# Performance work log

Hardware: AMD Instinct MI355X
Metric: run time of the kernel (lower is better)

Reference implementation:

```python
import jax, jax.numpy as jnp
import numpy as np

B, T, D, K = 8, 4096, 1024, 4096

def setup_inputs() -> dict:
    key = jax.random.key(0)
    kx, kc = jax.random.split(key)
    x = jax.random.normal(kx, (B, T, D), dtype=jnp.float32)
    C = jax.random.normal(kc, (D, K), dtype=jnp.float32)  # centroids stored as [d, K]
    Cnorm = jnp.sum(C * C, axis=0, keepdims=True)  # [1, K], matches torch precompute
    return {"x": x, "C": C, "Cnorm": Cnorm}

def reference(x, C, Cnorm):
    batched = x.ndim == 3
    if batched:
        b, t, d = x.shape
        x2 = x.reshape(-1, d)  # [N, d]
    else:
        x2 = x
    dist = jnp.sum(x2 * x2, axis=1, keepdims=True) - 2.0 * (x2 @ C) + Cnorm
    assigned = jnp.argmin(dist, axis=1)
    if batched:
        assigned = assigned.reshape(b, t)
    return assigned
```

## Files before the change

kernel.cpp:

```cpp
#include <hip/hip_runtime.h>
#include <cstdint>
#include <cstddef>

typedef _Float16 half8 __attribute__((ext_vector_type(8)));
typedef _Float16 half4 __attribute__((ext_vector_type(4)));
typedef float    floatx4 __attribute__((ext_vector_type(4)));

constexpr int N_ROWS = 32768;
constexpr int D_DIM  = 1024;
constexpr int K_CENT = 4096;
constexpr int CAP    = 4096;
constexpr int KSL    = 2;
constexpr int RSL    = 8;
constexpr float EPS_GAP = 0.4f;

__device__ __forceinline__ void gload_lds16(const void* g, void* l) {
    __builtin_amdgcn_global_load_lds(
        (const __attribute__((address_space(1))) uint32_t*)g,
        (__attribute__((address_space(3))) uint32_t*)l, 16, 0, 0);
}

__global__ __launch_bounds__(256) void convert_C_kernel(
    const float* __restrict__ C, _Float16* __restrict__ ChiT, _Float16* __restrict__ CloT)
{
    __shared__ float tile[32][33];
    const int bk = blockIdx.x, bd = blockIdx.y, t = threadIdx.x;
    const int r = t >> 3, c4 = (t & 7) * 4;
    const float4 v = *(const float4*)&C[(size_t)(bd * 32 + r) * K_CENT + bk * 32 + c4];
    tile[r][c4 + 0] = v.x; tile[r][c4 + 1] = v.y;
    tile[r][c4 + 2] = v.z; tile[r][c4 + 3] = v.w;
    __syncthreads();
    half4 h, l;
#pragma unroll
    for (int i = 0; i < 4; ++i) {
        const float f = tile[c4 + i][r];
        const _Float16 hi = (_Float16)f;
        h[i] = hi;
        l[i] = (_Float16)(f - (float)hi);
    }
    *(half4*)&ChiT[(size_t)(bk * 32 + r) * D_DIM + bd * 32 + c4] = h;
    *(half4*)&CloT[(size_t)(bk * 32 + r) * D_DIM + bd * 32 + c4] = l;
}

__global__ __launch_bounds__(256) void convert_x_kernel(
    const float* __restrict__ x, _Float16* __restrict__ xh)
{
    const size_t g = (size_t)blockIdx.x * 256 + threadIdx.x;
    const float4 v0 = *(const float4*)&x[g * 8];
    const float4 v1 = *(const float4*)&x[g * 8 + 4];
    half8 h;
    h[0] = (_Float16)v0.x; h[1] = (_Float16)v0.y; h[2] = (_Float16)v0.z; h[3] = (_Float16)v0.w;
    h[4] = (_Float16)v1.x; h[5] = (_Float16)v1.y; h[6] = (_Float16)v1.z; h[7] = (_Float16)v1.w;
    *(half8*)&xh[g * 8] = h;
}

constexpr int P_XH = 0;
constexpr int P_CH = 4096;
constexpr int P_HB = 12288;

__device__ __forceinline__ void stage6(
    _Float16* buf, const _Float16* __restrict__ xh, const _Float16* __restrict__ ChiT,
    int row0, int kc, int kd, int wid, int scol, int skg)
{
#pragma unroll
    for (int q = 0; q < 2; ++q) {
        const int sub = wid * 2 + q;
        gload_lds16(&xh[(size_t)(row0 + sub * 16 + scol) * D_DIM + kd + skg * 8],
                    buf + P_XH + sub * 512);
    }
#pragma unroll
    for (int q = 0; q < 4; ++q) {
        const int sub = wid * 4 + q;
        gload_lds16(&ChiT[(size_t)(kc + sub * 16 + scol) * D_DIM + kd + skg * 8],
                    buf + P_CH + sub * 512);
    }
}

__global__ __launch_bounds__(256, 2) void kmeans_pass1(
    const _Float16* __restrict__ xh, const _Float16* __restrict__ ChiT,
    const float* __restrict__ Cnorm,
    float* __restrict__ m1buf, int* __restrict__ i1buf, float* __restrict__ m2buf)
{
    __shared__ _Float16 lds[3][P_HB];
    __shared__ float red_d[2][64][2];
    __shared__ int   red_i[2][64][2];
    __shared__ float red_2[2][64][2];

    const int bid  = blockIdx.x;
    const int xcd  = bid & 7;
    const int ks   = xcd & 1;
    const int rb   = (bid >> 3) * 4 + (xcd >> 1);
    const int row0 = rb * 128;
    const int kb0  = ks * (K_CENT / KSL);

    const int tid  = threadIdx.x;
    const int lane = tid & 63;
    const int wid  = tid >> 6;
    const int wm   = wid >> 1;
    const int wn   = wid & 1;

    const int l15 = lane & 15;
    const int l4  = lane >> 4;
    const int kge = l4 ^ ((l15 >> 1) & 3);
    const int fragoff = l15 * 32 + kge * 8;

    const int scol = lane >> 2;
    const int skg  = (lane & 3) ^ ((scol >> 1) & 3);

    float rm1 = 3.4e38f, rm2 = 3.4e38f;
    int   ri1 = 0;

    constexpr int NSTEP = ((K_CENT / KSL) / 256) * 32;

    stage6(lds[0], xh, ChiT, row0, kb0, 0,  wid, scol, skg);
    stage6(lds[1], xh, ChiT, row0, kb0, 32, wid, scol, skg);

    floatx4 acc[4][8];
#pragma unroll
    for (int i = 0; i < 4; ++i)
#pragma unroll
        for (int j = 0; j < 8; ++j) acc[i][j] = (floatx4)0.0f;

    int cur = 0;
    for (int s = 0; s < NSTEP; ++s) {
        _Float16* bufc = lds[cur];
        const int s2 = s + 2;
        if (s2 < NSTEP) {
            const int nkc = kb0 + (s2 >> 5) * 256;
            const int nkd = (s2 & 31) * 32;
            const int b2  = (cur >= 1) ? cur - 1 : 2;
            stage6(lds[b2], xh, ChiT, row0, nkc, nkd, wid, scol, skg);
            asm volatile("s_waitcnt vmcnt(12)" ::: "memory");
        } else if (s + 1 < NSTEP) {
            asm volatile("s_waitcnt vmcnt(6)" ::: "memory");
        } else {
            asm volatile("s_waitcnt vmcnt(0)" ::: "memory");
        }
        __builtin_amdgcn_s_barrier();
        __builtin_amdgcn_sched_barrier(0);

        half8 ah[4], bh[8];
#pragma unroll
        for (int i = 0; i < 4; ++i)
            ah[i] = *(const half8*)(bufc + P_XH + (wm * 4 + i) * 512 + fragoff);
#pragma unroll
        for (int j = 0; j < 8; ++j)
            bh[j] = *(const half8*)(bufc + P_CH + (wn * 8 + j) * 512 + fragoff);

        __builtin_amdgcn_s_setprio(1);
#pragma unroll
        for (int i = 0; i < 4; ++i)
#pragma unroll
            for (int j = 0; j < 8; ++j)
                acc[i][j] = __builtin_amdgcn_mfma_f32_16x16x32_f16(ah[i], bh[j], acc[i][j], 0, 0, 0);
        __builtin_amdgcn_s_setprio(0);

        __builtin_amdgcn_sched_barrier(0);
        asm volatile("" ::: "memory");
        __builtin_amdgcn_s_barrier();

        cur = (cur == 2) ? 0 : cur + 1;

        if ((s & 31) == 31) {
            const int ci   = s >> 5;
            const int colw = ci * 256 + wn * 128;
            float cn8[8];
#pragma unroll
            for (int j = 0; j < 8; ++j) cn8[j] = Cnorm[kb0 + colw + j * 16 + l15];

#pragma unroll
            for (int i = 0; i < 4; ++i)
#pragma unroll
                for (int r = 0; r < 4; ++r) {
                    float m1 = 3.4e38f, m2 = 3.4e38f;
                    int   i1 = 0;
#pragma unroll
                    for (int j = 0; j < 8; ++j) {
                        const float d  = fmaf(-2.0f, acc[i][j][r], cn8[j]);
                        const int   ix = kb0 + colw + j * 16 + l15;
                        if (d < m1) { m2 = m1; m1 = d; i1 = ix; }
                        else if (d < m2) { m2 = d; }
                    }
#pragma unroll
                    for (int off = 1; off < 16; off <<= 1) {
                        const float om1 = __shfl_xor(m1, off, 64);
                        const int   oi  = __shfl_xor(i1, off, 64);
                        const float om2 = __shfl_xor(m2, off, 64);
                        const float nm2 = fminf(fminf(m2, om2), fmaxf(m1, om1));
                        if (om1 < m1 || (om1 == m1 && oi < i1)) { m1 = om1; i1 = oi; }
                        m2 = nm2;
                    }
                    if (l15 == 0) {
                        const int rr = i * 16 + l4 * 4 + r;
                        red_d[wm][rr][wn] = m1;
                        red_i[wm][rr][wn] = i1;
                        red_2[wm][rr][wn] = m2;
                    }
                }
            asm volatile("s_waitcnt lgkmcnt(0)" ::: "memory");
            __builtin_amdgcn_s_barrier();
            __builtin_amdgcn_sched_barrier(0);

            if (tid < 128) {
                const int hh = tid >> 7;
                const int rr = tid & 127;
                const int h2 = rr >> 6;
                const int r2 = rr & 63;
                float m1 = red_d[h2][r2][0], m2 = red_2[h2][r2][0];
                int   i1 = red_i[h2][r2][0];
                const float om1 = red_d[h2][r2][1];
                const int   oi  = red_i[h2][r2][1];
                const float om2 = red_2[h2][r2][1];
                m2 = fminf(fminf(m2, om2), fmaxf(m1, om1));
                if (om1 < m1 || (om1 == m1 && oi < i1)) { m1 = om1; i1 = oi; }
                const float nm2 = fminf(fminf(rm2, m2), fmaxf(rm1, m1));
                if (m1 < rm1 || (m1 == rm1 && i1 < ri1)) { rm1 = m1; ri1 = i1; }
                rm2 = nm2;
                (void)hh;
            }

#pragma unroll
            for (int i = 0; i < 4; ++i)
#pragma unroll
                for (int j = 0; j < 8; ++j) acc[i][j] = (floatx4)0.0f;
        }
    }

    if (tid < 128) {
        const size_t off = (size_t)ks * N_ROWS + row0 + tid;
        m1buf[off] = rm1;
        i1buf[off] = ri1;
        m2buf[off] = rm2;
    }
}

__global__ __launch_bounds__(256) void kmeans_merge4(
    const float* __restrict__ m1buf, const int* __restrict__ i1buf,
    const float* __restrict__ m2buf, int* __restrict__ out,
    int* __restrict__ urows, unsigned int* __restrict__ ucount)
{
    const int row = blockIdx.x * 256 + threadIdx.x;
    float m1 = m1buf[row], m2 = m2buf[row];
    int   i1 = i1buf[row];
#pragma unroll
    for (int s = 1; s < KSL; ++s) {
        const float om1 = m1buf[(size_t)s * N_ROWS + row];
        const float om2 = m2buf[(size_t)s * N_ROWS + row];
        const int   oi  = i1buf[(size_t)s * N_ROWS + row];
        const float nm2 = fminf(fminf(m2, om2), fmaxf(m1, om1));
        if (om1 < m1 || (om1 == m1 && oi < i1)) { m1 = om1; i1 = oi; }
        m2 = nm2;
    }
    out[row] = i1;
    if (m2 - m1 <= EPS_GAP) {
        const unsigned slot = atomicAdd(ucount, 1u);
        if (slot < (unsigned)CAP) urows[slot] = row;
    }
}

__global__ __launch_bounds__(64) void kmeans_gather(
    const float* __restrict__ x, const int* __restrict__ urows,
    const unsigned int* __restrict__ ucount,
    _Float16* __restrict__ xch, _Float16* __restrict__ xcl)
{
    const unsigned cntr = *ucount;
    const unsigned cnt = cntr > (unsigned)CAP ? (unsigned)CAP : cntr;
    const unsigned slot = blockIdx.x;
    if (slot >= cnt) return;
    const int row = urows[slot];
    const int t = threadIdx.x;
#pragma unroll
    for (int e = 0; e < 16; ++e) {
        const int idx = e * 64 + t;
        const float v = x[(size_t)row * D_DIM + idx];
        const _Float16 h = (_Float16)v;
        xch[(size_t)slot * D_DIM + idx] = h;
        xcl[(size_t)slot * D_DIM + idx] = (_Float16)(v - (float)h);
    }
}

constexpr int R_XH = 0;
constexpr int R_XL = 1024;
constexpr int R_CH = 2048;
constexpr int R_CL = 10240;
constexpr int R_HB = 18432;

__global__ __launch_bounds__(256) void kmeans_rescore2(
    const _Float16* __restrict__ xch, const _Float16* __restrict__ xcl,
    const _Float16* __restrict__ ChiT, const _Float16* __restrict__ CloT,
    const float* __restrict__ Cnorm, const unsigned int* __restrict__ ucount,
    float* __restrict__ rpd, int* __restrict__ rpi)
{
    const unsigned cntr = *ucount;
    const unsigned cnt = cntr > (unsigned)CAP ? (unsigned)CAP : cntr;
    const int bid = blockIdx.x;
    const int ksl = bid & 7;
    const int grp = bid >> 3;
    if ((unsigned)(grp * 32) >= cnt) return;

    __shared__ _Float16 lds[2][R_HB];
    __shared__ float rd[32][4];
    __shared__ int   ri[32][4];

    const int tid  = threadIdx.x;
    const int lane = tid & 63;
    const int wid  = tid >> 6;
    const int l15  = lane & 15;
    const int l4   = lane >> 4;
    const int kge  = l4 ^ ((l15 >> 1) & 3);
    const int fragoff = l15 * 32 + kge * 8;
    const int scol = lane >> 2;
    const int skg  = (lane & 3) ^ ((scol >> 1) & 3);

    const int base  = grp * 32;
    const int kbase = ksl * (K_CENT / RSL);

    float best[2][4];
    int   bidx[2][4];
#pragma unroll
    for (int i = 0; i < 2; ++i)
#pragma unroll
        for (int r = 0; r < 4; ++r) { best[i][r] = 3.4e38f; bidx[i][r] = 0; }

    for (int ch = 0; ch < 2; ++ch) {
        const int kc = kbase + ch * 256;
        floatx4 acc[2][4];
#pragma unroll
        for (int i = 0; i < 2; ++i)
#pragma unroll
            for (int j = 0; j < 4; ++j) acc[i][j] = (floatx4)0.0f;

        {
            _Float16* buf = lds[0];
#pragma unroll
            for (int q = 0; q < 4; ++q) {
                const int sub = wid * 4 + q;
                gload_lds16(&ChiT[(size_t)(kc + sub * 16 + scol) * D_DIM + 0 + skg * 8], buf + R_CH + sub * 512);
                gload_lds16(&CloT[(size_t)(kc + sub * 16 + scol) * D_DIM + 0 + skg * 8], buf + R_CL + sub * 512);
            }
            if (wid < 2)
                gload_lds16(&xch[(size_t)(base + wid * 16 + scol) * D_DIM + 0 + skg * 8], buf + R_XH + wid * 512);
            else
                gload_lds16(&xcl[(size_t)(base + (wid - 2) * 16 + scol) * D_DIM + 0 + skg * 8], buf + R_XL + (wid - 2) * 512);
            __syncthreads();
        }

        for (int kdi = 0; kdi < D_DIM / 32; ++kdi) {
            const int cur = kdi & 1;
            _Float16* bufc = lds[cur];
            _Float16* bufn = lds[cur ^ 1];
            const int  kdn = (kdi + 1) * 32;
            const bool pf  = (kdi + 1 < D_DIM / 32);

            if (pf) {
#pragma unroll
                for (int q = 0; q < 4; ++q) {
                    const int sub = wid * 4 + q;
                    gload_lds16(&ChiT[(size_t)(kc + sub * 16 + scol) * D_DIM + kdn + skg * 8], bufn + R_CH + sub * 512);
                    gload_lds16(&CloT[(size_t)(kc + sub * 16 + scol) * D_DIM + kdn + skg * 8], bufn + R_CL + sub * 512);
                }
                if (wid < 2)
                    gload_lds16(&xch[(size_t)(base + wid * 16 + scol) * D_DIM + kdn + skg * 8], bufn + R_XH + wid * 512);
                else
                    gload_lds16(&xcl[(size_t)(base + (wid - 2) * 16 + scol) * D_DIM + kdn + skg * 8], bufn + R_XL + (wid - 2) * 512);
            }

            half8 ah[2], al[2], bh[4], bl[4];
#pragma unroll
            for (int i = 0; i < 2; ++i) {
                ah[i] = *(const half8*)(bufc + R_XH + i * 512 + fragoff);
                al[i] = *(const half8*)(bufc + R_XL + i * 512 + fragoff);
            }
#pragma unroll
            for (int j = 0; j < 4; ++j) {
                bh[j] = *(const half8*)(bufc + R_CH + (wid * 4 + j) * 512 + fragoff);
                bl[j] = *(const half8*)(bufc + R_CL + (wid * 4 + j) * 512 + fragoff);
            }
#pragma unroll
            for (int i = 0; i < 2; ++i)
#pragma unroll
                for (int j = 0; j < 4; ++j) {
                    acc[i][j] = __builtin_amdgcn_mfma_f32_16x16x32_f16(ah[i], bh[j], acc[i][j], 0, 0, 0);
                    acc[i][j] = __builtin_amdgcn_mfma_f32_16x16x32_f16(ah[i], bl[j], acc[i][j], 0, 0, 0);
                    acc[i][j] = __builtin_amdgcn_mfma_f32_16x16x32_f16(al[i], bh[j], acc[i][j], 0, 0, 0);
                }
            __syncthreads();
        }

#pragma unroll
        for (int j = 0; j < 4; ++j) {
            const int col = kc + wid * 64 + j * 16 + l15;
            const float cn = Cnorm[col];
#pragma unroll
            for (int i = 0; i < 2; ++i)
#pragma unroll
                for (int r = 0; r < 4; ++r) {
                    const float d = fmaf(-2.0f, acc[i][j][r], cn);
                    if (d < best[i][r]) { best[i][r] = d; bidx[i][r] = col; }
                }
        }
    }

#pragma unroll
    for (int i = 0; i < 2; ++i)
#pragma unroll
        for (int r = 0; r < 4; ++r) {
            float m1 = best[i][r];
            int   i1 = bidx[i][r];
#pragma unroll
            for (int off = 1; off < 16; off <<= 1) {
                const float om1 = __shfl_xor(m1, off, 64);
                const int   oi  = __shfl_xor(i1, off, 64);
                if (om1 < m1 || (om1 == m1 && oi < i1)) { m1 = om1; i1 = oi; }
            }
            if (l15 == 0) { rd[i * 16 + l4 * 4 + r][wid] = m1; ri[i * 16 + l4 * 4 + r][wid] = i1; }
        }
    __syncthreads();

    if (tid < 32) {
        float m1 = rd[tid][0];
        int   i1 = ri[tid][0];
#pragma unroll
        for (int w = 1; w < 4; ++w) {
            const float om1 = rd[tid][w];
            const int   oi  = ri[tid][w];
            if (om1 < m1 || (om1 == m1 && oi < i1)) { m1 = om1; i1 = oi; }
        }
        rpd[(size_t)(base + tid) * RSL + ksl] = m1;
        rpi[(size_t)(base + tid) * RSL + ksl] = i1;
    }
}

__global__ __launch_bounds__(256) void kmeans_merge2(
    const float* __restrict__ rpd, const int* __restrict__ rpi,
    const int* __restrict__ urows, const unsigned int* __restrict__ ucount,
    int* __restrict__ out)
{
    const unsigned cntr = *ucount;
    const unsigned cnt = cntr > (unsigned)CAP ? (unsigned)CAP : cntr;
    const unsigned s = blockIdx.x * 256 + threadIdx.x;
    if (s >= cnt) return;
    float m1 = rpd[(size_t)s * RSL];
    int   i1 = rpi[(size_t)s * RSL];
#pragma unroll
    for (int k = 1; k < RSL; ++k) {
        const float om = rpd[(size_t)s * RSL + k];
        const int   oi = rpi[(size_t)s * RSL + k];
        if (om < m1 || (om == m1 && oi < i1)) { m1 = om; i1 = oi; }
    }
    out[urows[s]] = i1;
}

constexpr int F_XH = 0, F_XL = 4096, F_CH = 8192, F_CL = 16384, F_HB = 24576;

__device__ __forceinline__ void write_x2(_Float16* buf, const float4 v, int r, int kb) {
    const _Float16 h0 = (_Float16)v.x, h1 = (_Float16)v.y;
    const _Float16 h2 = (_Float16)v.z, h3 = (_Float16)v.w;
    const int kg  = kb >> 3;
    const int hs  = (kb >> 2) & 1;
    const int kge = kg ^ ((r >> 1) & 3);
    const int base = (r >> 4) * 512 + (r & 15) * 32 + kge * 8 + hs * 4;
    *(half4*)(buf + F_XH + base) = (half4){h0, h1, h2, h3};
    *(half4*)(buf + F_XL + base) = (half4){(_Float16)(v.x - (float)h0), (_Float16)(v.y - (float)h1),
                                           (_Float16)(v.z - (float)h2), (_Float16)(v.w - (float)h3)};
}

__global__ __launch_bounds__(512, 2) void kmeans_mfma_kernel(
    const float* __restrict__ x, const _Float16* __restrict__ ChiT,
    const _Float16* __restrict__ CloT, const float* __restrict__ Cnorm,
    int* __restrict__ out)
{
    __shared__ _Float16 lds[2][F_HB];
    __shared__ float red_d[2][64][4];
    __shared__ int   red_i[2][64][4];

    const int tid  = threadIdx.x;
    const int lane = tid & 63;
    const int wid  = tid >> 6;
    const int wm   = wid >> 2;
    const int wn   = wid & 3;
    const int row0 = blockIdx.x * 128;
    const int l15 = lane & 15;
    const int l4  = lane >> 4;
    const int kge = l4 ^ ((l15 >> 1) & 3);
    const int fragoff = l15 * 32 + kge * 8;
    const int sr = tid >> 2, sc = tid & 3;
    const int ccol = lane >> 2;
    const int ckg  = (lane & 3) ^ ((ccol >> 1) & 3);

    float best[4][4];
    int   bidx[4][4];
#pragma unroll
    for (int i = 0; i < 4; ++i)
#pragma unroll
        for (int r = 0; r < 4; ++r) { best[i][r] = 3.4e38f; bidx[i][r] = 0; }

    for (int kc = 0; kc < K_CENT; kc += 256) {
        floatx4 acc[4][4];
#pragma unroll
        for (int i = 0; i < 4; ++i)
#pragma unroll
            for (int j = 0; j < 4; ++j) acc[i][j] = (floatx4)0.0f;
        {
            _Float16* buf = lds[0];
            const float4 xv0 = *(const float4*)&x[(size_t)(row0 + sr) * D_DIM + 0 + sc * 4];
            const float4 xv1 = *(const float4*)&x[(size_t)(row0 + sr) * D_DIM + 16 + sc * 4];
            gload_lds16(&ChiT[(size_t)(kc + wid * 16 + ccol) * D_DIM + 0 + ckg * 8], buf + F_CH + wid * 512);
            gload_lds16(&ChiT[(size_t)(kc + (wid + 8) * 16 + ccol) * D_DIM + 0 + ckg * 8], buf + F_CH + (wid + 8) * 512);
            gload_lds16(&CloT[(size_t)(kc + wid * 16 + ccol) * D_DIM + 0 + ckg * 8], buf + F_CL + wid * 512);
            gload_lds16(&CloT[(size_t)(kc + (wid + 8) * 16 + ccol) * D_DIM + 0 + ckg * 8], buf + F_CL + (wid + 8) * 512);
            write_x2(buf, xv0, sr, sc * 4);
            write_x2(buf, xv1, sr, sc * 4 + 16);
            __syncthreads();
        }
        for (int kdi = 0; kdi < D_DIM / 32; ++kdi) {
            const int cur = kdi & 1;
            _Float16* bufc = lds[cur];
            _Float16* bufn = lds[cur ^ 1];
            const int  kdn = (kdi + 1) * 32;
            const bool pf  = (kdi + 1 < D_DIM / 32);
            float4 xv0, xv1;
            if (pf) {
                xv0 = *(const float4*)&x[(size_t)(row0 + sr) * D_DIM + kdn + sc * 4];
                xv1 = *(const float4*)&x[(size_t)(row0 + sr) * D_DIM + kdn + 16 + sc * 4];
                gload_lds16(&ChiT[(size_t)(kc + wid * 16 + ccol) * D_DIM + kdn + ckg * 8], bufn + F_CH + wid * 512);
                gload_lds16(&ChiT[(size_t)(kc + (wid + 8) * 16 + ccol) * D_DIM + kdn + ckg * 8], bufn + F_CH + (wid + 8) * 512);
                gload_lds16(&CloT[(size_t)(kc + wid * 16 + ccol) * D_DIM + kdn + ckg * 8], bufn + F_CL + wid * 512);
                gload_lds16(&CloT[(size_t)(kc + (wid + 8) * 16 + ccol) * D_DIM + kdn + ckg * 8], bufn + F_CL + (wid + 8) * 512);
            }
            half8 ah[4], al[4], bh[4], bl[4];
#pragma unroll
            for (int i = 0; i < 4; ++i) {
                ah[i] = *(const half8*)(bufc + F_XH + (wm * 4 + i) * 512 + fragoff);
                al[i] = *(const half8*)(bufc + F_XL + (wm * 4 + i) * 512 + fragoff);
            }
#pragma unroll
            for (int j = 0; j < 4; ++j) {
                bh[j] = *(const half8*)(bufc + F_CH + (wn * 4 + j) * 512 + fragoff);
                bl[j] = *(const half8*)(bufc + F_CL + (wn * 4 + j) * 512 + fragoff);
            }
#pragma unroll
            for (int i = 0; i < 4; ++i)
#pragma unroll
                for (int j = 0; j < 4; ++j) {
                    acc[i][j] = __builtin_amdgcn_mfma_f32_16x16x32_f16(ah[i], bh[j], acc[i][j], 0, 0, 0);
                    acc[i][j] = __builtin_amdgcn_mfma_f32_16x16x32_f16(ah[i], bl[j], acc[i][j], 0, 0, 0);
                    acc[i][j] = __builtin_amdgcn_mfma_f32_16x16x32_f16(al[i], bh[j], acc[i][j], 0, 0, 0);
                }
            if (pf) {
                write_x2(bufn, xv0, sr, sc * 4);
                write_x2(bufn, xv1, sr, sc * 4 + 16);
            }
            __syncthreads();
        }
        const int colw = kc + wn * 64;
#pragma unroll
        for (int ns = 0; ns < 4; ++ns) {
            const float cn = Cnorm[colw + ns * 16 + l15];
            const int   ix = colw + ns * 16 + l15;
#pragma unroll
            for (int i = 0; i < 4; ++i)
#pragma unroll
                for (int r = 0; r < 4; ++r) {
                    const float d = fmaf(-2.0f, acc[i][ns][r], cn);
                    if (d < best[i][r]) { best[i][r] = d; bidx[i][r] = ix; }
                }
        }
    }
#pragma unroll
    for (int i = 0; i < 4; ++i)
#pragma unroll
        for (int r = 0; r < 4; ++r) {
            float d  = best[i][r];
            int   ix = bidx[i][r];
#pragma unroll
            for (int off = 1; off < 16; off <<= 1) {
                const float od = __shfl_xor(d, off, 64);
                const int   oi = __shfl_xor(ix, off, 64);
                if (od < d || (od == d && oi < ix)) { d = od; ix = oi; }
            }
            if (l15 == 0) {
                red_d[wm][i * 16 + l4 * 4 + r][wn] = d;
                red_i[wm][i * 16 + l4 * 4 + r][wn] = ix;
            }
        }
    __syncthreads();
    if (tid < 128) {
        const int hh = tid >> 6, rr = tid & 63;
        float bd = red_d[hh][rr][0];
        int   bi2 = red_i[hh][rr][0];
#pragma unroll
        for (int w = 1; w < 4; ++w) {
            const float od = red_d[hh][rr][w];
            const int   oi = red_i[hh][rr][w];
            if (od < bd || (od == bd && oi < bi2)) { bd = od; bi2 = oi; }
        }
        out[row0 + tid] = bi2;
    }
}

__global__ __launch_bounds__(256, 2) void kmeans_assign_f32(
    const float* __restrict__ x, const float* __restrict__ Cm,
    const float* __restrict__ Cnorm, int* __restrict__ out)
{
    __shared__ float xs[32][64];
    __shared__ float cs[32][64];
    const int tid = threadIdx.x;
    const int tx = tid & 15, ty = tid >> 4;
    const int row0 = blockIdx.x * 64;
    const int xr = tid >> 3, xc = tid & 7;
    const int cr = tid >> 4, cc = tid & 15;
    float best[4]; int bidx[4];
#pragma unroll
    for (int i = 0; i < 4; ++i) { best[i] = 3.4e38f; bidx[i] = 0; }
    for (int kc = 0; kc < K_CENT; kc += 64) {
        float acc[16];
#pragma unroll
        for (int i = 0; i < 16; ++i) acc[i] = 0.0f;
        for (int kd = 0; kd < D_DIM; kd += 32) {
            const float4 xv0 = *(const float4*)&x[(size_t)(row0 + xr) * D_DIM + kd + xc * 4];
            const float4 xv1 = *(const float4*)&x[(size_t)(row0 + xr + 32) * D_DIM + kd + xc * 4];
            const float4 cv0 = *(const float4*)&Cm[(size_t)(kd + cr) * K_CENT + kc + cc * 4];
            const float4 cv1 = *(const float4*)&Cm[(size_t)(kd + cr + 16) * K_CENT + kc + cc * 4];
            __syncthreads();
            xs[xc*4+0][xr] = xv0.x; xs[xc*4+1][xr] = xv0.y; xs[xc*4+2][xr] = xv0.z; xs[xc*4+3][xr] = xv0.w;
            xs[xc*4+0][xr+32] = xv1.x; xs[xc*4+1][xr+32] = xv1.y; xs[xc*4+2][xr+32] = xv1.z; xs[xc*4+3][xr+32] = xv1.w;
            *(float4*)&cs[cr][cc*4]    = cv0;
            *(float4*)&cs[cr+16][cc*4] = cv1;
            __syncthreads();
#pragma unroll
            for (int kk = 0; kk < 32; ++kk) {
                const float4 a = *(const float4*)&xs[kk][ty*4];
                const float4 b = *(const float4*)&cs[kk][tx*4];
                acc[ 0] += a.x*b.x; acc[ 1] += a.x*b.y; acc[ 2] += a.x*b.z; acc[ 3] += a.x*b.w;
                acc[ 4] += a.y*b.x; acc[ 5] += a.y*b.y; acc[ 6] += a.y*b.z; acc[ 7] += a.y*b.w;
                acc[ 8] += a.z*b.x; acc[ 9] += a.z*b.y; acc[10] += a.z*b.z; acc[11] += a.z*b.w;
                acc[12] += a.w*b.x; acc[13] += a.w*b.y; acc[14] += a.w*b.z; acc[15] += a.w*b.w;
            }
        }
        const float4 cn = *(const float4*)&Cnorm[kc + tx*4];
        const float cnv[4] = {cn.x, cn.y, cn.z, cn.w};
#pragma unroll
        for (int i = 0; i < 4; ++i)
#pragma unroll
            for (int j = 0; j < 4; ++j) {
                const float dist = cnv[j] - 2.0f * acc[i*4+j];
                const int   idx  = kc + tx*4 + j;
                if (dist < best[i]) { best[i] = dist; bidx[i] = idx; }
            }
    }
#pragma unroll
    for (int i = 0; i < 4; ++i) {
        float d = best[i]; int ix = bidx[i];
#pragma unroll
        for (int off = 1; off < 16; off <<= 1) {
            const float od = __shfl_xor(d, off, 64);
            const int   oi = __shfl_xor(ix, off, 64);
            if (od < d || (od == d && oi < ix)) { d = od; ix = oi; }
        }
        if (tx == 0) out[row0 + ty*4 + i] = ix;
    }
}

extern "C" void kernel_launch(void* const* d_in, const int* in_sizes, int n_in,
                              void* d_out, int out_size, void* d_ws, size_t ws_size,
                              hipStream_t stream) {
    const float* x     = (const float*)d_in[0];
    const float* C     = (const float*)d_in[1];
    const float* Cnorm = (const float*)d_in[2];
    int* out = (int*)d_out;

    const size_t chalf = (size_t)K_CENT * D_DIM;
    const size_t capd  = (size_t)CAP * D_DIM;
    const size_t xhN   = (size_t)N_ROWS * D_DIM;

    const size_t sz_base = (2 * chalf + 2 * capd) * 2
                         + (size_t)KSL * N_ROWS * 12
                         + (size_t)CAP * RSL * 8
                         + (size_t)CAP * 4 + 64;
    const size_t need_full = sz_base + xhN * 2;
    const size_t need_r3   = 2 * chalf * 2;

    if (ws_size >= need_full) {
        _Float16* ChiT = (_Float16*)d_ws;
        _Float16* CloT = ChiT + chalf;
        _Float16* xch  = CloT + chalf;
        _Float16* xcl  = xch + capd;
        float* m1buf = (float*)(xcl + capd);
        float* m2buf = m1buf + (size_t)KSL * N_ROWS;
        int*   i1buf = (int*)(m2buf + (size_t)KSL * N_ROWS);
        float* rpd   = (float*)(i1buf + (size_t)KSL * N_ROWS);
        int*   rpi   = (int*)(rpd + (size_t)CAP * RSL);
        int*   urows = rpi + (size_t)CAP * RSL;
        unsigned int* ucount = (unsigned int*)(urows + CAP);
        _Float16* xh = (_Float16*)(ucount + 16);

        convert_C_kernel<<<dim3(128, 32), 256, 0, stream>>>(C, ChiT, CloT);
        convert_x_kernel<<<dim3((int)(xhN / 2048)), 256, 0, stream>>>(x, xh);
        hipMemsetAsync(ucount, 0, sizeof(unsigned int), stream);
        kmeans_pass1<<<dim3(256 * KSL), 256, 0, stream>>>(xh, ChiT, Cnorm, m1buf, i1buf, m2buf);
        kmeans_merge4<<<dim3(N_ROWS / 256), 256, 0, stream>>>(m1buf, i1buf, m2buf, out, urows, ucount);
        kmeans_gather<<<dim3(CAP), 64, 0, stream>>>(x, urows, ucount, xch, xcl);
        kmeans_rescore2<<<dim3((CAP / 32) * RSL), 256, 0, stream>>>(xch, xcl, ChiT, CloT, Cnorm, ucount, rpd, rpi);
        kmeans_merge2<<<dim3(CAP / 256), 256, 0, stream>>>(rpd, rpi, urows, ucount, out);
    } else if (ws_size >= need_r3) {
        _Float16* ChiT = (_Float16*)d_ws;
        _Float16* CloT = ChiT + chalf;
        convert_C_kernel<<<dim3(128, 32), 256, 0, stream>>>(C, ChiT, CloT);
        kmeans_mfma_kernel<<<dim3(N_ROWS / 128), 512, 0, stream>>>(x, ChiT, CloT, Cnorm, out);
    } else {
        kmeans_assign_f32<<<dim3(N_ROWS / 64), 256, 0, stream>>>(x, C, Cnorm, out);
    }
}
```

Baseline: 476.2 us.

## Enlarge pass1 tile to 256x256 with 8 waves and split-phase staging

The first-pass GEMM kernel now uses 512-thread blocks, each covering 256 rows by 256 centroids per chunk, with 8 waves arranged 2x4 and each wave computing 128x64. The MFMA work per step is split into two halves. The x-tile and C-tile global-to-LDS loads are issued in separate phases between those halves, so loads overlap with compute. The larger tile raises arithmetic intensity and cuts redundant global/LDS traffic per output. In exchange there are more barriers per step, larger LDS use (three 32KB buffers), and half as many blocks (256), which may underfill the GPU.

Result: slower. 509.4 us (+7.0%).

```diff
diff --git a/kernel.cpp b/kernel.cpp
--- a/kernel.cpp
+++ b/kernel.cpp
@@ -54,50 +54,55 @@
     *(half8*)&xh[g * 8] = h;
 }
 
-constexpr int P_XH = 0;
-constexpr int P_CH = 4096;
-constexpr int P_HB = 12288;
-
-__device__ __forceinline__ void stage6(
-    _Float16* buf, const _Float16* __restrict__ xh, const _Float16* __restrict__ ChiT,
-    int row0, int kc, int kd, int wid, int scol, int skg)
+constexpr int P8_B  = 8192;
+constexpr int P8_HB = 16384;
+
+__device__ __forceinline__ void stageA8(
+    _Float16* buf, const _Float16* __restrict__ xh,
+    int row0, int kd, int wid, int scol, int skg)
 {
 #pragma unroll
     for (int q = 0; q < 2; ++q) {
         const int sub = wid * 2 + q;
         gload_lds16(&xh[(size_t)(row0 + sub * 16 + scol) * D_DIM + kd + skg * 8],
-                    buf + P_XH + sub * 512);
-    }
-#pragma unroll
-    for (int q = 0; q < 4; ++q) {
-        const int sub = wid * 4 + q;
+                    buf + sub * 512);
+    }
+}
+
+__device__ __forceinline__ void stageB8(
+    _Float16* buf, const _Float16* __restrict__ ChiT,
+    int kc, int kd, int wid, int scol, int skg)
+{
+#pragma unroll
+    for (int q = 0; q < 2; ++q) {
+        const int sub = wid * 2 + q;
         gload_lds16(&ChiT[(size_t)(kc + sub * 16 + scol) * D_DIM + kd + skg * 8],
-                    buf + P_CH + sub * 512);
-    }
-}
-
-__global__ __launch_bounds__(256, 2) void kmeans_pass1(
+                    buf + P8_B + sub * 512);
+    }
+}
+
+__global__ __launch_bounds__(512, 2) void kmeans_pass1(
     const _Float16* __restrict__ xh, const _Float16* __restrict__ ChiT,
     const float* __restrict__ Cnorm,
     float* __restrict__ m1buf, int* __restrict__ i1buf, float* __restrict__ m2buf)
 {
-    __shared__ _Float16 lds[3][P_HB];
-    __shared__ float red_d[2][64][2];
-    __shared__ int   red_i[2][64][2];
-    __shared__ float red_2[2][64][2];
+    __shared__ _Float16 lds[3][P8_HB];
+    __shared__ float red_d[256][4];
+    __shared__ int   red_i[256][4];
+    __shared__ float red_2[256][4];
 
     const int bid  = blockIdx.x;
     const int xcd  = bid & 7;
     const int ks   = xcd & 1;
     const int rb   = (bid >> 3) * 4 + (xcd >> 1);
-    const int row0 = rb * 128;
+    const int row0 = rb * 256;
     const int kb0  = ks * (K_CENT / KSL);
 
     const int tid  = threadIdx.x;
     const int lane = tid & 63;
     const int wid  = tid >> 6;
-    const int wm   = wid >> 1;
-    const int wn   = wid & 1;
+    const int wm   = wid >> 2;
+    const int wn   = wid & 3;
 
     const int l15 = lane & 15;
     const int l4  = lane >> 4;
@@ -110,123 +115,138 @@
     float rm1 = 3.4e38f, rm2 = 3.4e38f;
     int   ri1 = 0;
 
-    constexpr int NSTEP = ((K_CENT / KSL) / 256) * 32;
-
-    stage6(lds[0], xh, ChiT, row0, kb0, 0,  wid, scol, skg);
-    stage6(lds[1], xh, ChiT, row0, kb0, 32, wid, scol, skg);
-
-    floatx4 acc[4][8];
-#pragma unroll
-    for (int i = 0; i < 4; ++i)
-#pragma unroll
-        for (int j = 0; j < 8; ++j) acc[i][j] = (floatx4)0.0f;
+    constexpr int NCH   = (K_CENT / KSL) / 256;
+    constexpr int NSTEP = NCH * 32;
+
+    stageA8(lds[0], xh,   row0, 0,  wid, scol, skg);
+    stageB8(lds[0], ChiT, kb0,  0,  wid, scol, skg);
+    stageA8(lds[1], xh,   row0, 32, wid, scol, skg);
+    stageB8(lds[1], ChiT, kb0,  32, wid, scol, skg);
+    asm volatile("s_waitcnt vmcnt(4)" ::: "memory");
+    __builtin_amdgcn_s_barrier();
 
     int cur = 0;
-    for (int s = 0; s < NSTEP; ++s) {
-        _Float16* bufc = lds[cur];
-        const int s2 = s + 2;
-        if (s2 < NSTEP) {
-            const int nkc = kb0 + (s2 >> 5) * 256;
-            const int nkd = (s2 & 31) * 32;
-            const int b2  = (cur >= 1) ? cur - 1 : 2;
-            stage6(lds[b2], xh, ChiT, row0, nkc, nkd, wid, scol, skg);
-            asm volatile("s_waitcnt vmcnt(12)" ::: "memory");
-        } else if (s + 1 < NSTEP) {
-            asm volatile("s_waitcnt vmcnt(6)" ::: "memory");
-        } else {
-            asm volatile("s_waitcnt vmcnt(0)" ::: "memory");
-        }
+    int sg  = 0;
+
+    for (int ci = 0; ci < NCH; ++ci) {
+        floatx4 acc[8][4];
+#pragma unroll
+        for (int i = 0; i < 8; ++i)
+#pragma unroll
+            for (int j = 0; j < 4; ++j) acc[i][j] = (floatx4)0.0f;
+
+        for (int kdi = 0; kdi < 32; ++kdi, ++sg) {
+            _Float16* bufc = lds[cur];
+            const int  nb  = (cur == 0) ? 2 : cur - 1;
+            const int  s2  = sg + 2;
+            const bool st  = (s2 < NSTEP);
+            const int  kc2 = kb0 + (s2 >> 5) * 256;
+            const int  kd2 = (s2 & 31) * 32;
+
+            half8 ah[4], bh[4];
+#pragma unroll
+            for (int i = 0; i < 4; ++i)
+                ah[i] = *(const half8*)(bufc + (wm * 8 + i) * 512 + fragoff);
+#pragma unroll
+            for (int j = 0; j < 4; ++j)
+                bh[j] = *(const half8*)(bufc + P8_B + (wn * 4 + j) * 512 + fragoff);
+            if (st) stageA8(lds[nb], xh, row0, kd2, wid, scol, skg);
+
+            __builtin_amdgcn_s_barrier();
+            asm volatile("s_waitcnt lgkmcnt(0)" ::: "memory");
+            __builtin_amdgcn_sched_barrier(0);
+            __builtin_amdgcn_s_setprio(1);
+#pragma unroll
+            for (int i = 0; i < 4; ++i)
+#pragma unroll
+                for (int j = 0; j < 4; ++j)
+                    acc[i][j] = __builtin_amdgcn_mfma_f32_16x16x32_f16(ah[i], bh[j], acc[i][j], 0, 0, 0);
+            __builtin_amdgcn_s_setprio(0);
+            __builtin_amdgcn_sched_barrier(0);
+            __builtin_amdgcn_s_barrier();
+
+            half8 ah2[4];
+#pragma unroll
+            for (int i = 0; i < 4; ++i)
+                ah2[i] = *(const half8*)(bufc + (wm * 8 + 4 + i) * 512 + fragoff);
+            if (st) {
+                stageB8(lds[nb], ChiT, kc2, kd2, wid, scol, skg);
+                asm volatile("s_waitcnt vmcnt(4)" ::: "memory");
+            } else {
+                asm volatile("s_waitcnt vmcnt(0)" ::: "memory");
+            }
+            __builtin_amdgcn_s_barrier();
+            asm volatile("s_waitcnt lgkmcnt(0)" ::: "memory");
+            __builtin_amdgcn_sched_barrier(0);
+            __builtin_amdgcn_s_setprio(1);
+#pragma unroll
+            for (int i = 0; i < 4; ++i)
+#pragma unroll
+                for (int j = 0; j < 4; ++j)
+                    acc[4 + i][j] = __builtin_amdgcn_mfma_f32_16x16x32_f16(ah2[i], bh[j], acc[4 + i][j], 0, 0, 0);
+            __builtin_amdgcn_s_setprio(0);
+            __builtin_amdgcn_sched_barrier(0);
+            __builtin_amdgcn_s_barrier();
+
+            cur = (cur == 2) ? 0 : cur + 1;
+        }
+
+        const int colw = ci * 256 + wn * 64;
+        float cn4[4];
+#pragma unroll
+        for (int j = 0; j < 4; ++j) cn4[j] = Cnorm[kb0 + colw + j * 16 + l15];
+
+#pragma unroll
+        for (int i = 0; i < 8; ++i)
+#pragma unroll
+            for (int r = 0; r < 4; ++r) {
+                float m1 = 3.4e38f, m2 = 3.4e38f;
+                int   i1 = 0;
+#pragma unroll
+                for (int j = 0; j < 4; ++j) {
+                    const float d  = fmaf(-2.0f, acc[i][j][r], cn4[j]);
+                    const int   ix = kb0 + colw + j * 16 + l15;
+                    if (d < m1) { m2 = m1; m1 = d; i1 = ix; }
+                    else if (d < m2) { m2 = d; }
+                }
+#pragma unroll
+                for (int off = 1; off < 16; off <<= 1) {
+                    const float om1 = __shfl_xor(m1, off, 64);
+                    const int   oi  = __shfl_xor(i1, off, 64);
+                    const float om2 = __shfl_xor(m2, off, 64);
+                    const float nm2 = fminf(fminf(m2, om2), fmaxf(m1, om1));
+                    if (om1 < m1 || (om1 == m1 && oi < i1)) { m1 = om1; i1 = oi; }
+                    m2 = nm2;
+                }
+                if (l15 == 0) {
+                    const int rr = wm * 128 + i * 16 + l4 * 4 + r;
+                    red_d[rr][wn] = m1;
+                    red_i[rr][wn] = i1;
+                    red_2[rr][wn] = m2;
+                }
+            }
+        asm volatile("s_waitcnt lgkmcnt(0)" ::: "memory");
         __builtin_amdgcn_s_barrier();
         __builtin_amdgcn_sched_barrier(0);
 
-        half8 ah[4], bh[8];
-#pragma unroll
-        for (int i = 0; i < 4; ++i)
-            ah[i] = *(const half8*)(bufc + P_XH + (wm * 4 + i) * 512 + fragoff);
-#pragma unroll
-        for (int j = 0; j < 8; ++j)
-            bh[j] = *(const half8*)(bufc + P_CH + (wn * 8 + j) * 512 + fragoff);
-
-        __builtin_amdgcn_s_setprio(1);
-#pragma unroll
-        for (int i = 0; i < 4; ++i)
-#pragma unroll
-            for (int j = 0; j < 8; ++j)
-                acc[i][j] = __builtin_amdgcn_mfma_f32_16x16x32_f16(ah[i], bh[j], acc[i][j], 0, 0, 0);
-        __builtin_amdgcn_s_setprio(0);
-
-        __builtin_amdgcn_sched_barrier(0);
-        asm volatile("" ::: "memory");
-        __builtin_amdgcn_s_barrier();
-
-        cur = (cur == 2) ? 0 : cur + 1;
-
-        if ((s & 31) == 31) {
-            const int ci   = s >> 5;
-            const int colw = ci * 256 + wn * 128;
-            float cn8[8];
-#pragma unroll
-            for (int j = 0; j < 8; ++j) cn8[j] = Cnorm[kb0 + colw + j * 16 + l15];
-
-#pragma unroll
-            for (int i = 0; i < 4; ++i)
-#pragma unroll
-                for (int r = 0; r < 4; ++r) {
-                    float m1 = 3.4e38f, m2 = 3.4e38f;
-                    int   i1 = 0;
-#pragma unroll
-                    for (int j = 0; j < 8; ++j) {
-                        const float d  = fmaf(-2.0f, acc[i][j][r], cn8[j]);
-                        const int   ix = kb0 + colw + j * 16 + l15;
-                        if (d < m1) { m2 = m1; m1 = d; i1 = ix; }
-                        else if (d < m2) { m2 = d; }
-                    }
-#pragma unroll
-                    for (int off = 1; off < 16; off <<= 1) {
-                        const float om1 = __shfl_xor(m1, off, 64);
-                        const int   oi  = __shfl_xor(i1, off, 64);
-                        const float om2 = __shfl_xor(m2, off, 64);
-                        const float nm2 = fminf(fminf(m2, om2), fmaxf(m1, om1));
-                        if (om1 < m1 || (om1 == m1 && oi < i1)) { m1 = om1; i1 = oi; }
-                        m2 = nm2;
-                    }
-                    if (l15 == 0) {
-                        const int rr = i * 16 + l4 * 4 + r;
-                        red_d[wm][rr][wn] = m1;
-                        red_i[wm][rr][wn] = i1;
-                        red_2[wm][rr][wn] = m2;
-                    }
-                }
-            asm volatile("s_waitcnt lgkmcnt(0)" ::: "memory");
-            __builtin_amdgcn_s_barrier();
-            __builtin_amdgcn_sched_barrier(0);
-
-            if (tid < 128) {
-                const int hh = tid >> 7;
-                const int rr = tid & 127;
-                const int h2 = rr >> 6;
-                const int r2 = rr & 63;
-                float m1 = red_d[h2][r2][0], m2 = red_2[h2][r2][0];
-                int   i1 = red_i[h2][r2][0];
-                const float om1 = red_d[h2][r2][1];
-                const int   oi  = red_i[h2][r2][1];
-                const float om2 = red_2[h2][r2][1];
+        if (tid < 256) {
+            float m1 = red_d[tid][0], m2 = red_2[tid][0];
+            int   i1 = red_i[tid][0];
+#pragma unroll
+            for (int w = 1; w < 4; ++w) {
+                const float om1 = red_d[tid][w];
+                const int   oi  = red_i[tid][w];
+                const float om2 = red_2[tid][w];
                 m2 = fminf(fminf(m2, om2), fmaxf(m1, om1));
                 if (om1 < m1 || (om1 == m1 && oi < i1)) { m1 = om1; i1 = oi; }
-                const float nm2 = fminf(fminf(rm2, m2), fmaxf(rm1, m1));
-                if (m1 < rm1 || (m1 == rm1 && i1 < ri1)) { rm1 = m1; ri1 = i1; }
-                rm2 = nm2;
-                (void)hh;
-            }
-
-#pragma unroll
-            for (int i = 0; i < 4; ++i)
-#pragma unroll
-                for (int j = 0; j < 8; ++j) acc[i][j] = (floatx4)0.0f;
-        }
-    }
-
-    if (tid < 128) {
+            }
+            const float nm2 = fminf(fminf(rm2, m2), fmaxf(rm1, m1));
+            if (m1 < rm1 || (m1 == rm1 && i1 < ri1)) { rm1 = m1; ri1 = i1; }
+            rm2 = nm2;
+        }
+    }
+
+    if (tid < 256) {
         const size_t off = (size_t)ks * N_ROWS + row0 + tid;
         m1buf[off] = rm1;
         i1buf[off] = ri1;
@@ -698,7 +718,7 @@
         convert_C_kernel<<<dim3(128, 32), 256, 0, stream>>>(C, ChiT, CloT);
         convert_x_kernel<<<dim3((int)(xhN / 2048)), 256, 0, stream>>>(x, xh);
         hipMemsetAsync(ucount, 0, sizeof(unsigned int), stream);
-        kmeans_pass1<<<dim3(256 * KSL), 256, 0, stream>>>(xh, ChiT, Cnorm, m1buf, i1buf, m2buf);
+        kmeans_pass1<<<dim3(128 * KSL), 512, 0, stream>>>(xh, ChiT, Cnorm, m1buf, i1buf, m2buf);
         kmeans_merge4<<<dim3(N_ROWS / 256), 256, 0, stream>>>(m1buf, i1buf, m2buf, out, urows, ucount);
         kmeans_gather<<<dim3(CAP), 64, 0, stream>>>(x, urows, ucount, xch, xcl);
         kmeans_rescore2<<<dim3((CAP / 32) * RSL), 256, 0, stream>>>(xch, xcl, ChiT, CloT, Cnorm, ucount, rpd, rpi);
```

## Shrink pass1 tile to 128x128, split K into four slices, double-buffer

Applied to the files above, without the earlier changes.

The pass-1 GEMM+argmin kernel now uses a 128x128 output tile instead of 128x256 and splits the centroid dimension into four slices instead of two. The three-stage LDS pipeline becomes two-stage, and occupancy is raised to three blocks per CU. This is meant to add parallelism and occupancy through smaller accumulators and less LDS per block. In exchange each x tile is reloaded more often relative to the compute, per-block arithmetic intensity drops, and prefetch depth is reduced to one stage. The merge step must also combine four slices rather than two.

Result: slower. 501.8 us (+5.4%).

```diff
diff --git a/kernel.cpp b/kernel.cpp
--- a/kernel.cpp
+++ b/kernel.cpp
@@ -10,7 +10,7 @@
 constexpr int D_DIM  = 1024;
 constexpr int K_CENT = 4096;
 constexpr int CAP    = 4096;
-constexpr int KSL    = 2;
+constexpr int KSL    = 4;
 constexpr int RSL    = 8;
 constexpr float EPS_GAP = 0.4f;
 
@@ -54,11 +54,11 @@
     *(half8*)&xh[g * 8] = h;
 }
 
-constexpr int P_XH = 0;
-constexpr int P_CH = 4096;
-constexpr int P_HB = 12288;
-
-__device__ __forceinline__ void stage6(
+constexpr int Q_A  = 0;
+constexpr int Q_B  = 4096;
+constexpr int Q_HB = 8192;
+
+__device__ __forceinline__ void stage4(
     _Float16* buf, const _Float16* __restrict__ xh, const _Float16* __restrict__ ChiT,
     int row0, int kc, int kd, int wid, int scol, int skg)
 {
@@ -66,30 +66,30 @@
     for (int q = 0; q < 2; ++q) {
         const int sub = wid * 2 + q;
         gload_lds16(&xh[(size_t)(row0 + sub * 16 + scol) * D_DIM + kd + skg * 8],
-                    buf + P_XH + sub * 512);
-    }
-#pragma unroll
-    for (int q = 0; q < 4; ++q) {
-        const int sub = wid * 4 + q;
+                    buf + Q_A + sub * 512);
+    }
+#pragma unroll
+    for (int q = 0; q < 2; ++q) {
+        const int sub = wid * 2 + q;
         gload_lds16(&ChiT[(size_t)(kc + sub * 16 + scol) * D_DIM + kd + skg * 8],
-                    buf + P_CH + sub * 512);
-    }
-}
-
-__global__ __launch_bounds__(256, 2) void kmeans_pass1(
+                    buf + Q_B + sub * 512);
+    }
+}
+
+__global__ __launch_bounds__(256, 3) void kmeans_pass1(
     const _Float16* __restrict__ xh, const _Float16* __restrict__ ChiT,
     const float* __restrict__ Cnorm,
     float* __restrict__ m1buf, int* __restrict__ i1buf, float* __restrict__ m2buf)
 {
-    __shared__ _Float16 lds[3][P_HB];
+    __shared__ _Float16 lds[2][Q_HB];
     __shared__ float red_d[2][64][2];
     __shared__ int   red_i[2][64][2];
     __shared__ float red_2[2][64][2];
 
     const int bid  = blockIdx.x;
     const int xcd  = bid & 7;
-    const int ks   = xcd & 1;
-    const int rb   = (bid >> 3) * 4 + (xcd >> 1);
+    const int ks   = xcd & 3;
+    const int rb   = (bid >> 3) * 2 + (xcd >> 2);
     const int row0 = rb * 128;
     const int kb0  = ks * (K_CENT / KSL);
 
@@ -110,63 +110,56 @@
     float rm1 = 3.4e38f, rm2 = 3.4e38f;
     int   ri1 = 0;
 
-    constexpr int NSTEP = ((K_CENT / KSL) / 256) * 32;
-
-    stage6(lds[0], xh, ChiT, row0, kb0, 0,  wid, scol, skg);
-    stage6(lds[1], xh, ChiT, row0, kb0, 32, wid, scol, skg);
-
-    floatx4 acc[4][8];
+    constexpr int NCH   = (K_CENT / KSL) / 128;
+    constexpr int NSTEP = NCH * 32;
+
+    stage4(lds[0], xh, ChiT, row0, kb0, 0, wid, scol, skg);
+
+    floatx4 acc[4][4];
 #pragma unroll
     for (int i = 0; i < 4; ++i)
 #pragma unroll
-        for (int j = 0; j < 8; ++j) acc[i][j] = (floatx4)0.0f;
-
-    int cur = 0;
+        for (int j = 0; j < 4; ++j) acc[i][j] = (floatx4)0.0f;
+
     for (int s = 0; s < NSTEP; ++s) {
-        _Float16* bufc = lds[cur];
-        const int s2 = s + 2;
-        if (s2 < NSTEP) {
-            const int nkc = kb0 + (s2 >> 5) * 256;
-            const int nkd = (s2 & 31) * 32;
-            const int b2  = (cur >= 1) ? cur - 1 : 2;
-            stage6(lds[b2], xh, ChiT, row0, nkc, nkd, wid, scol, skg);
-            asm volatile("s_waitcnt vmcnt(12)" ::: "memory");
-        } else if (s + 1 < NSTEP) {
-            asm volatile("s_waitcnt vmcnt(6)" ::: "memory");
+        _Float16* bufc = lds[s & 1];
+        _Float16* bufn = lds[(s + 1) & 1];
+        const int s1 = s + 1;
+        if (s1 < NSTEP) {
+            const int nkc = kb0 + (s1 >> 5) * 128;
+            const int nkd = (s1 & 31) * 32;
+            stage4(bufn, xh, ChiT, row0, nkc, nkd, wid, scol, skg);
+            asm volatile("s_waitcnt vmcnt(4)" ::: "memory");
         } else {
             asm volatile("s_waitcnt vmcnt(0)" ::: "memory");
         }
         __builtin_amdgcn_s_barrier();
-        __builtin_amdgcn_sched_barrier(0);
-
-        half8 ah[4], bh[8];
+
+        half8 ah[4], bh[4];
 #pragma unroll
         for (int i = 0; i < 4; ++i)
-            ah[i] = *(const half8*)(bufc + P_XH + (wm * 4 + i) * 512 + fragoff);
-#pragma unroll
-        for (int j = 0; j < 8; ++j)
-            bh[j] = *(const half8*)(bufc + P_CH + (wn * 8 + j) * 512 + fragoff);
+            ah[i] = *(const half8*)(bufc + Q_A + (wm * 4 + i) * 512 + fragoff);
+#pragma unroll
+        for (int j = 0; j < 4; ++j)
+            bh[j] = *(const half8*)(bufc + Q_B + (wn * 4 + j) * 512 + fragoff);
 
         __builtin_amdgcn_s_setprio(1);
 #pragma unroll
         for (int i = 0; i < 4; ++i)
 #pragma unroll
-            for (int j = 0; j < 8; ++j)
+            for (int j = 0; j < 4; ++j)
                 acc[i][j] = __builtin_amdgcn_mfma_f32_16x16x32_f16(ah[i], bh[j], acc[i][j], 0, 0, 0);
         __builtin_amdgcn_s_setprio(0);
 
-        __builtin_amdgcn_sched_barrier(0);
         asm volatile("" ::: "memory");
         __builtin_amdgcn_s_barrier();
 
-        cur = (cur == 2) ? 0 : cur + 1;
-
         if ((s & 31) == 31) {
             const int ci   = s >> 5;
-            const int colw = ci * 256 + wn * 128;
-            float cn8[8];
-#pragma unroll
-            for (int j = 0; j < 8; ++j) cn8[j] = Cnorm[kb0 + colw + j * 16 + l15];
+            const int colw = ci * 128 + wn * 64;
+            float cn4[4];
+#pragma unroll
+            for (int j = 0; j < 4; ++j) cn4[j] = Cnorm[kb0 + colw + j * 16 + l15];
 
 #pragma unroll
             for (int i = 0; i < 4; ++i)
@@ -175,8 +168,8 @@
                     float m1 = 3.4e38f, m2 = 3.4e38f;
                     int   i1 = 0;
 #pragma unroll
-                    for (int j = 0; j < 8; ++j) {
-                        const float d  = fmaf(-2.0f, acc[i][j][r], cn8[j]);
+                    for (int j = 0; j < 4; ++j) {
+                        const float d  = fmaf(-2.0f, acc[i][j][r], cn4[j]);
                         const int   ix = kb0 + colw + j * 16 + l15;
                         if (d < m1) { m2 = m1; m1 = d; i1 = ix; }
                         else if (d < m2) { m2 = d; }
@@ -202,10 +195,8 @@
             __builtin_amdgcn_sched_barrier(0);
 
             if (tid < 128) {
-                const int hh = tid >> 7;
-                const int rr = tid & 127;
-                const int h2 = rr >> 6;
-                const int r2 = rr & 63;
+                const int h2 = tid >> 6;
+                const int r2 = tid & 63;
                 float m1 = red_d[h2][r2][0], m2 = red_2[h2][r2][0];
                 int   i1 = red_i[h2][r2][0];
                 const float om1 = red_d[h2][r2][1];
@@ -216,13 +207,12 @@
                 const float nm2 = fminf(fminf(rm2, m2), fmaxf(rm1, m1));
                 if (m1 < rm1 || (m1 == rm1 && i1 < ri1)) { rm1 = m1; ri1 = i1; }
                 rm2 = nm2;
-                (void)hh;
             }
 
 #pragma unroll
             for (int i = 0; i < 4; ++i)
 #pragma unroll
-                for (int j = 0; j < 8; ++j) acc[i][j] = (floatx4)0.0f;
+                for (int j = 0; j < 4; ++j) acc[i][j] = (floatx4)0.0f;
         }
     }
 
```
